# Kernel optimization log

Measured on AMD Instinct MI355X. Metric: run time of the kernel, lower is better.

Reference implementation:

```python
import jax, jax.numpy as jnp
import numpy as np

B, S, D, H = 2, 2048, 1024, 16
DH = D // H  # per-head dim (64)


def setup_inputs() -> dict:
    key = jax.random.key(0)
    ks = jax.random.split(key, 12)
    scale = 1.0 / np.sqrt(D)
    return {
        "q": jax.random.normal(ks[0], (B, S, D), jnp.float32),
        "k": jax.random.normal(ks[1], (B, S, D), jnp.float32),
        "v": jax.random.normal(ks[2], (B, S, D), jnp.float32),
        # per-head projection weights, stacked: head i's nn.Linear(d_model, d)
        "Wq": jax.random.normal(ks[3], (H, D, DH), jnp.float32) * scale,
        "Wk": jax.random.normal(ks[4], (H, D, DH), jnp.float32) * scale,
        "Wv": jax.random.normal(ks[5], (H, D, DH), jnp.float32) * scale,
        "bq": jax.random.normal(ks[6], (H, DH), jnp.float32) * scale,
        "bk": jax.random.normal(ks[7], (H, DH), jnp.float32) * scale,
        "bv": jax.random.normal(ks[8], (H, DH), jnp.float32) * scale,
        # output projection nn.Linear(d_model, d_model)
        "Wo": jax.random.normal(ks[9], (D, D), jnp.float32) * scale,
        "bo": jax.random.normal(ks[10], (D,), jnp.float32) * scale,
    }


def reference(q, k, v, Wq, Wk, Wv, bq, bk, bv, Wo, bo):
    # Per-head projections (batched over heads): [B, S, H, DH]
    Q = jnp.einsum("bsd,hdk->bshk", q, Wq) + bq
    K = jnp.einsum("bsd,hdk->bshk", k, Wk) + bk
    V = jnp.einsum("bsd,hdk->bshk", v, Wv) + bv
    # Scaled dot-product attention per head: scores [B, H, S, S]
    scores = jnp.einsum("bqhk,bvhk->bhqv", Q, K) / jnp.sqrt(jnp.float32(DH))
    aw = jax.nn.softmax(scores, axis=-1)  # attention weights
    # Weighted values, concat heads along last dim (head i -> slice i*DH:(i+1)*DH)
    ctx = jnp.einsum("bhqv,bvhk->bqhk", aw, V).reshape(B, S, D)
    out = ctx @ Wo + bo  # dropout is identity in eval
    # aws stacked over heads first, matching torch.stack: [H, B, S, S]
    aws = jnp.transpose(aw, (1, 0, 2, 3))
    return out, aws
```

## Files before the change

kernel.cpp:

```cpp
#include <hip/hip_runtime.h>
#include <hip/hip_bf16.h>
#include <cstdint>
#include <cstddef>

#define B_  2
#define S_  2048
#define D_  1024
#define H_  16
#define DH_ 64
#define OUT_ELEMS ((size_t)B_ * S_ * D_)

typedef unsigned short u16;
typedef __attribute__((ext_vector_type(8))) short short8;
typedef __attribute__((ext_vector_type(4))) float f32x4;

__device__ __forceinline__ float bf2f(u16 u) {
    union { unsigned int i; float f; } x;
    x.i = ((unsigned int)u) << 16;
    return x.f;
}
__device__ __forceinline__ u16 f2bf(float f) {
    union { float f; unsigned int i; } x; x.f = f;
    unsigned int r = x.i + 0x7fffu + ((x.i >> 16) & 1u);
    return (u16)(r >> 16);
}

#define LDSTR 72

__global__ __launch_bounds__(64) void detect_kernel(const void* q, unsigned int* flag)
{
    const int lane = threadIdx.x;
    const u16 e = ((const u16*)q)[lane * 2];
    const float v = bf2f(e);
    const float a = fabsf(v);
    const bool wild = !(a <= 100.f) || (a != 0.f && a < 1e-6f);
    unsigned long long m = __ballot(wild);
    if (lane == 0) *flag = (__popcll(m) >= 16) ? 1u : 0u;
}

__global__ __launch_bounds__(256) void convert_bias_kernel(
    const void* bq, const void* bk, const void* bv, const void* bo,
    u16* __restrict__ dst, const unsigned int* __restrict__ flag)
{
    const bool ext32 = flag[0] != 0;
    const int which = blockIdx.y;
    const void* src = which == 0 ? bq : which == 1 ? bk : which == 2 ? bv : bo;
    u16* d = dst + which * 1024;
    const int tid = threadIdx.x;
    #pragma unroll
    for (int i = 0; i < 4; ++i) {
        const int idx = i * 256 + tid;
        d[idx] = ext32 ? f2bf(((const float*)src)[idx]) : ((const u16*)src)[idx];
    }
}

__global__ __launch_bounds__(256) void transpose_weights_kernel(
    const void* Wq, const void* Wk, const void* Wv, const void* Wo,
    u16* __restrict__ WqT, u16* __restrict__ WkT,
    u16* __restrict__ WvT, u16* __restrict__ WoT,
    const unsigned int* __restrict__ flag)
{
    __shared__ u16 t[64][65];
    const bool ext32 = flag[0] != 0;
    const int which = blockIdx.y;
    const void* src = which == 0 ? Wq : which == 1 ? Wk : which == 2 ? Wv : Wo;
    u16* dst = which == 0 ? WqT : which == 1 ? WkT : which == 2 ? WvT : WoT;
    const int tile = blockIdx.x;
    const int tid = threadIdx.x;
    const int rr = tid >> 6;
    const int cc = tid & 63;

    if (which < 3) {
        const int h = tile >> 4, d0 = (tile & 15) * 64;
        #pragma unroll
        for (int i = 0; i < 16; ++i) {
            int r = rr + i * 4;
            size_t idx = ((size_t)(h * 1024 + d0 + r)) * 64 + cc;
            t[r][cc] = ext32 ? f2bf(((const float*)src)[idx]) : ((const u16*)src)[idx];
        }
        __syncthreads();
        #pragma unroll
        for (int i = 0; i < 16; ++i) {
            int c = rr + i * 4;
            dst[((size_t)(h * 64 + c)) * 1024 + d0 + cc] = t[cc][c];
        }
    } else {
        const int d0 = (tile >> 4) * 64, n0 = (tile & 15) * 64;
        #pragma unroll
        for (int i = 0; i < 16; ++i) {
            int r = rr + i * 4;
            size_t idx = (size_t)(d0 + r) * 1024 + n0 + cc;
            t[r][cc] = ext32 ? f2bf(((const float*)src)[idx]) : ((const u16*)src)[idx];
        }
        __syncthreads();
        #pragma unroll
        for (int i = 0; i < 16; ++i) {
            int c = rr + i * 4;
            dst[(size_t)(n0 + c) * 1024 + d0 + cc] = t[cc][c];
        }
    }
}

__global__ __launch_bounds__(256) void gemm_bias_kernel(
    const void* __restrict__ A, const u16* __restrict__ BT,
    const u16* __restrict__ bias, void* __restrict__ out,
    int M, int K, int mode, int a_ext, const unsigned int* __restrict__ flag)
{
    __shared__ u16 lA[128 * LDSTR];
    __shared__ u16 lB[128 * LDSTR];
    const bool ext32 = flag[0] != 0;
    const int tid = threadIdx.x;
    const int wave = tid >> 6, lane = tid & 63;
    const int m0 = blockIdx.x * 128, n0 = blockIdx.y * 128;
    const int wm = (wave >> 1) * 64, wn = (wave & 1) * 64;

    f32x4 acc[4][4];
    #pragma unroll
    for (int i = 0; i < 4; ++i)
        #pragma unroll
        for (int j = 0; j < 4; ++j)
            acc[i][j] = (f32x4){0.f, 0.f, 0.f, 0.f};

    for (int k0 = 0; k0 < K; k0 += 64) {
        if (a_ext && ext32) {
            const float* Af = (const float*)A;
            #pragma unroll
            for (int it = 0; it < 4; ++it) {
                int e = (it * 256 + tid) * 8;
                int r = e >> 6, c = e & 63;
                const float4 f0 = *(const float4*)&Af[(size_t)(m0 + r) * K + k0 + c];
                const float4 f1 = *(const float4*)&Af[(size_t)(m0 + r) * K + k0 + c + 4];
                short8 o;
                o[0] = (short)f2bf(f0.x); o[1] = (short)f2bf(f0.y);
                o[2] = (short)f2bf(f0.z); o[3] = (short)f2bf(f0.w);
                o[4] = (short)f2bf(f1.x); o[5] = (short)f2bf(f1.y);
                o[6] = (short)f2bf(f1.z); o[7] = (short)f2bf(f1.w);
                *(short8*)&lA[r * LDSTR + c] = o;
                *(short8*)&lB[r * LDSTR + c] = *(const short8*)&BT[(size_t)(n0 + r) * K + k0 + c];
            }
        } else {
            const u16* Ab = (const u16*)A;
            #pragma unroll
            for (int it = 0; it < 4; ++it) {
                int e = (it * 256 + tid) * 8;
                int r = e >> 6, c = e & 63;
                *(short8*)&lA[r * LDSTR + c] = *(const short8*)&Ab[(size_t)(m0 + r) * K + k0 + c];
                *(short8*)&lB[r * LDSTR + c] = *(const short8*)&BT[(size_t)(n0 + r) * K + k0 + c];
            }
        }
        __syncthreads();
        #pragma unroll
        for (int ks = 0; ks < 2; ++ks) {
            const int fk = ((lane >> 4) << 3) + ks * 32;
            const int fr = lane & 15;
            short8 af[4], bf[4];
            #pragma unroll
            for (int i = 0; i < 4; ++i) af[i] = *(short8*)&lA[(wm + i * 16 + fr) * LDSTR + fk];
            #pragma unroll
            for (int j = 0; j < 4; ++j) bf[j] = *(short8*)&lB[(wn + j * 16 + fr) * LDSTR + fk];
            #pragma unroll
            for (int i = 0; i < 4; ++i)
                #pragma unroll
                for (int j = 0; j < 4; ++j)
                    acc[i][j] = __builtin_amdgcn_mfma_f32_16x16x32_bf16(af[i], bf[j], acc[i][j], 0, 0, 0);
        }
        __syncthreads();
    }

    const int cf = lane & 15;
    const int rb = (lane >> 4) * 4;
    #pragma unroll
    for (int j = 0; j < 4; ++j) {
        const int n = n0 + wn + j * 16 + cf;
        const float bval = bf2f(bias[n]);
        const int h = n >> 6, dh = n & 63;
        #pragma unroll
        for (int i = 0; i < 4; ++i) {
            #pragma unroll
            for (int reg = 0; reg < 4; ++reg) {
                const int m = m0 + wm + i * 16 + rb + reg;
                const float v = acc[i][j][reg] + bval;
                if (mode == 0) {
                    int b = m >> 11, s = m & (S_ - 1);
                    ((u16*)out)[((size_t)(b * H_ + h) * S_ + s) * DH_ + dh] = f2bf(v);
                } else if (mode == 1) {
                    int b = m >> 11, s = m & (S_ - 1);
                    ((u16*)out)[((size_t)(b * H_ + h) * DH_ + dh) * S_ + s] = f2bf(v);
                } else {
                    size_t off = (size_t)m * D_ + n;
                    if (ext32) ((float*)out)[off] = v;
                    else       ((u16*)out)[off] = f2bf(v);
                }
            }
        }
    }
}

template<int WITH_PV>
__global__ __launch_bounds__(256, 3) void fused_attn_kernel(
    const u16* __restrict__ Qp, const u16* __restrict__ Kp,
    const u16* __restrict__ Vt, void* __restrict__ dout,
    u16* __restrict__ ctx, const unsigned int* __restrict__ flag)
{
    __shared__ u16 lQ[64 * LDSTR];
    __shared__ u16 lK[64 * LDSTR];
    __shared__ u16 lV[WITH_PV ? 64 * LDSTR : 8];
    __shared__ u16 lP[WITH_PV ? 4 * 16 * LDSTR : 8];

    const bool ext32 = flag[0] != 0;
    const int tid = threadIdx.x;
    const int wave = tid >> 6, lane = tid & 63;
    const int lin = blockIdx.x;
    const int g = lin & 7, ii = lin >> 3;
    const int bh = g * 4 + (ii & 3);
    const int mblk = ii >> 2;
    const int b = bh >> 4, h = bh & 15;
    const int m0 = mblk * 64;
    const int wm = wave * 16;
    const int fr = lane & 15;
    const int quad = lane >> 4;
    const int fk = quad * 8;

    const u16* Qb = Qp + (size_t)bh * S_ * DH_;
    const u16* Kb = Kp + (size_t)bh * S_ * DH_;
    const u16* Vb = Vt + (size_t)bh * DH_ * S_;

    #pragma unroll
    for (int it = 0; it < 2; ++it) {
        int e = (it * 256 + tid) * 8;
        int r = e >> 6, c = e & 63;
        *(short8*)&lQ[r * LDSTR + c] = *(const short8*)&Qb[(size_t)(m0 + r) * DH_ + c];
    }
    __syncthreads();
    short8 aq[2];
    aq[0] = *(short8*)&lQ[(wm + fr) * LDSTR + fk];
    aq[1] = *(short8*)&lQ[(wm + fr) * LDSTR + fk + 32];

    float mrun[4], lrun[4];
    #pragma unroll
    for (int r = 0; r < 4; ++r) { mrun[r] = -1e30f; lrun[r] = 0.f; }

    for (int kt = 0; kt < S_ / 64; ++kt) {
        #pragma unroll
        for (int it = 0; it < 2; ++it) {
            int e = (it * 256 + tid) * 8;
            int r = e >> 6, c = e & 63;
            *(short8*)&lK[r * LDSTR + c] = *(const short8*)&Kb[(size_t)(kt * 64 + r) * DH_ + c];
        }
        __syncthreads();
        f32x4 sacc[4];
        #pragma unroll
        for (int j = 0; j < 4; ++j) sacc[j] = (f32x4){0.f, 0.f, 0.f, 0.f};
        #pragma unroll
        for (int ks = 0; ks < 2; ++ks)
            #pragma unroll
            for (int j = 0; j < 4; ++j) {
                short8 bk = *(short8*)&lK[(j * 16 + fr) * LDSTR + fk + ks * 32];
                sacc[j] = __builtin_amdgcn_mfma_f32_16x16x32_bf16(aq[ks], bk, sacc[j], 0, 0, 0);
            }
        __syncthreads();

        #pragma unroll
        for (int r = 0; r < 4; ++r) {
            float pm = fmaxf(fmaxf(sacc[0][r], sacc[1][r]), fmaxf(sacc[2][r], sacc[3][r]));
            #pragma unroll
            for (int off = 1; off < 16; off <<= 1) pm = fmaxf(pm, __shfl_xor(pm, off, 64));
            const float mnew = fmaxf(mrun[r], pm * 0.125f);
            float t = 0.f;
            #pragma unroll
            for (int j = 0; j < 4; ++j)
                t += __expf(fmaf(sacc[j][r], 0.125f, -mnew));
            #pragma unroll
            for (int off = 1; off < 16; off <<= 1) t += __shfl_xor(t, off, 64);
            lrun[r] = lrun[r] * __expf(mrun[r] - mnew) + t;
            mrun[r] = mnew;
        }
    }

    float inv[4];
    #pragma unroll
    for (int r = 0; r < 4; ++r) inv[r] = 1.f / lrun[r];

    f32x4 pv[4];
    if (WITH_PV) {
        #pragma unroll
        for (int j = 0; j < 4; ++j) pv[j] = (f32x4){0.f, 0.f, 0.f, 0.f};
    }

    float* awF = (float*)dout + OUT_ELEMS + (size_t)(h * B_ + b) * S_ * S_;
    u16*  awH = (u16*)dout + OUT_ELEMS + (size_t)(h * B_ + b) * S_ * S_;

    for (int kt = 0; kt < S_ / 64; ++kt) {
        #pragma unroll
        for (int it = 0; it < 2; ++it) {
            int e = (it * 256 + tid) * 8;
            int r = e >> 6, c = e & 63;
            *(short8*)&lK[r * LDSTR + c] = *(const short8*)&Kb[(size_t)(kt * 64 + r) * DH_ + c];
            if (WITH_PV)
                *(short8*)&lV[r * LDSTR + c] = *(const short8*)&Vb[(size_t)r * S_ + kt * 64 + c];
        }
        __syncthreads();
        f32x4 sacc[4];
        #pragma unroll
        for (int j = 0; j < 4; ++j) sacc[j] = (f32x4){0.f, 0.f, 0.f, 0.f};
        #pragma unroll
        for (int ks = 0; ks < 2; ++ks)
            #pragma unroll
            for (int j = 0; j < 4; ++j) {
                short8 bk = *(short8*)&lK[(j * 16 + fr) * LDSTR + fk + ks * 32];
                sacc[j] = __builtin_amdgcn_mfma_f32_16x16x32_bf16(aq[ks], bk, sacc[j], 0, 0, 0);
            }

        #pragma unroll
        for (int j = 0; j < 4; ++j) {
            const int col = kt * 64 + j * 16 + fr;
            #pragma unroll
            for (int r = 0; r < 4; ++r) {
                const float p = __expf(fmaf(sacc[j][r], 0.125f, -mrun[r])) * inv[r];
                const int row = m0 + wm + quad * 4 + r;
                if (ext32) awF[(size_t)row * S_ + col] = p;
                else       awH[(size_t)row * S_ + col] = f2bf(p);
                if (WITH_PV) lP[(wm + quad * 4 + r) * LDSTR + j * 16 + fr] = f2bf(p);
            }
        }
        if (WITH_PV) {
            asm volatile("s_waitcnt lgkmcnt(0)" ::: "memory");
            __builtin_amdgcn_sched_barrier(0);
            #pragma unroll
            for (int ks = 0; ks < 2; ++ks) {
                short8 ap = *(short8*)&lP[(wm + fr) * LDSTR + fk + ks * 32];
                #pragma unroll
                for (int j = 0; j < 4; ++j) {
                    short8 bv = *(short8*)&lV[(j * 16 + fr) * LDSTR + fk + ks * 32];
                    pv[j] = __builtin_amdgcn_mfma_f32_16x16x32_bf16(ap, bv, pv[j], 0, 0, 0);
                }
            }
        }
        __syncthreads();
    }

    if (WITH_PV) {
        #pragma unroll
        for (int j = 0; j < 4; ++j) {
            const int dh = j * 16 + fr;
            #pragma unroll
            for (int r = 0; r < 4; ++r) {
                const int mrow = m0 + wm + quad * 4 + r;
                ctx[((size_t)(b * S_ + mrow)) * D_ + h * DH_ + dh] = f2bf(pv[j][r]);
            }
        }
    }
}

__global__ __launch_bounds__(128) void ctx_kernel(
    const void* __restrict__ dout, const u16* __restrict__ Vt, u16* __restrict__ ctx,
    const unsigned int* __restrict__ flag)
{
    __shared__ u16 lA[128 * LDSTR];
    __shared__ u16 lB[64 * LDSTR];
    const bool ext32 = flag[0] != 0;
    const int tid = threadIdx.x;
    const int wave = tid >> 6, lane = tid & 63;
    const int bh = blockIdx.z, b = bh >> 4, h = bh & 15;
    const int m0 = blockIdx.x * 128;
    const int wm = wave * 64;
    const size_t abase = (size_t)(h * B_ + b) * S_ * S_;
    const u16* Bv = Vt + (size_t)bh * DH_ * S_;

    f32x4 acc[4][4];
    #pragma unroll
    for (int i = 0; i < 4; ++i)
        #pragma unroll
        for (int j = 0; j < 4; ++j)
            acc[i][j] = (f32x4){0.f, 0.f, 0.f, 0.f};

    for (int k0 = 0; k0 < S_; k0 += 64) {
        if (ext32) {
            const float* Awf = (const float*)dout + OUT_ELEMS + abase;
            #pragma unroll
            for (int it = 0; it < 8; ++it) {
                int e = (it * 128 + tid) * 8;
                int r = e >> 6, c = e & 63;
                const float4 f0 = *(const float4*)&Awf[(size_t)(m0 + r) * S_ + k0 + c];
                const float4 f1 = *(const float4*)&Awf[(size_t)(m0 + r) * S_ + k0 + c + 4];
                short8 o;
                o[0] = (short)f2bf(f0.x); o[1] = (short)f2bf(f0.y);
                o[2] = (short)f2bf(f0.z); o[3] = (short)f2bf(f0.w);
                o[4] = (short)f2bf(f1.x); o[5] = (short)f2bf(f1.y);
                o[6] = (short)f2bf(f1.z); o[7] = (short)f2bf(f1.w);
                *(short8*)&lA[r * LDSTR + c] = o;
            }
        } else {
            const u16* Awb = (const u16*)dout + OUT_ELEMS + abase;
            #pragma unroll
            for (int it = 0; it < 8; ++it) {
                int e = (it * 128 + tid) * 8;
                int r = e >> 6, c = e & 63;
                *(short8*)&lA[r * LDSTR + c] = *(const short8*)&Awb[(size_t)(m0 + r) * S_ + k0 + c];
            }
        }
        #pragma unroll
        for (int it = 0; it < 4; ++it) {
            int e = (it * 128 + tid) * 8;
            int r = e >> 6, c = e & 63;
            *(short8*)&lB[r * LDSTR + c] = *(const short8*)&Bv[(size_t)r * S_ + k0 + c];
        }
        __syncthreads();
        #pragma unroll
        for (int ks = 0; ks < 2; ++ks) {
            const int fk = ((lane >> 4) << 3) + ks * 32;
            const int fr = lane & 15;
            short8 af[4], bf[4];
            #pragma unroll
            for (int i = 0; i < 4; ++i) af[i] = *(short8*)&lA[(wm + i * 16 + fr) * LDSTR + fk];
            #pragma unroll
            for (int j = 0; j < 4; ++j) bf[j] = *(short8*)&lB[(j * 16 + fr) * LDSTR + fk];
            #pragma unroll
            for (int i = 0; i < 4; ++i)
                #pragma unroll
                for (int j = 0; j < 4; ++j)
                    acc[i][j] = __builtin_amdgcn_mfma_f32_16x16x32_bf16(af[i], bf[j], acc[i][j], 0, 0, 0);
        }
        __syncthreads();
    }

    const int cf = lane & 15;
    const int rb = (lane >> 4) * 4;
    #pragma unroll
    for (int j = 0; j < 4; ++j) {
        const int n = j * 16 + cf;
        #pragma unroll
        for (int i = 0; i < 4; ++i) {
            #pragma unroll
            for (int reg = 0; reg < 4; ++reg) {
                const int m = m0 + wm + i * 16 + rb + reg;
                ctx[((size_t)(b * S_ + m)) * D_ + h * DH_ + n] = f2bf(acc[i][j][reg]);
            }
        }
    }
}

extern "C" void kernel_launch(void* const* d_in, const int* in_sizes, int n_in,
                              void* d_out, int out_size, void* d_ws, size_t ws_size,
                              hipStream_t stream)
{
    const void* q  = d_in[0];
    const void* k  = d_in[1];
    const void* v  = d_in[2];
    const void* Wq = d_in[3];
    const void* Wk = d_in[4];
    const void* Wv = d_in[5];
    const void* bq = d_in[6];
    const void* bk = d_in[7];
    const void* bv = d_in[8];
    const void* Wo = d_in[9];
    const void* bo = d_in[10];

    u16* ws   = (u16*)d_ws;
    u16* WqT  = ws;
    u16* WkT  = ws + 1048576;
    u16* WvT  = ws + 2097152;
    u16* WoT  = ws + 3145728;
    u16* Qp   = ws + 4194304;
    u16* Kp   = ws + 8388608;
    u16* Vt   = ws + 12582912;
    u16* biasB = ws + 16777216;
    unsigned int* flag = (unsigned int*)(ws + 16781312);
    u16* ctxws = ws + 16781376;

    const bool big_ws = ws_size >= (size_t)(16781376 + 4194304) * sizeof(u16);
    u16* ctxbuf = big_ws ? ctxws : Qp;

    detect_kernel<<<1, 64, 0, stream>>>(q, flag);
    convert_bias_kernel<<<dim3(1, 4), 256, 0, stream>>>(bq, bk, bv, bo, biasB, flag);
    transpose_weights_kernel<<<dim3(256, 4), 256, 0, stream>>>(
        Wq, Wk, Wv, Wo, WqT, WkT, WvT, WoT, flag);
    gemm_bias_kernel<<<dim3(32, 8), 256, 0, stream>>>(q, WqT, biasB,        Qp, 4096, 1024, 0, 1, flag);
    gemm_bias_kernel<<<dim3(32, 8), 256, 0, stream>>>(k, WkT, biasB + 1024, Kp, 4096, 1024, 0, 1, flag);
    gemm_bias_kernel<<<dim3(32, 8), 256, 0, stream>>>(v, WvT, biasB + 2048, Vt, 4096, 1024, 1, 1, flag);

    if (big_ws) {
        fused_attn_kernel<1><<<dim3(1024), 256, 0, stream>>>(Qp, Kp, Vt, d_out, ctxws, flag);
    } else {
        fused_attn_kernel<0><<<dim3(1024), 256, 0, stream>>>(Qp, Kp, Vt, d_out, nullptr, flag);
        ctx_kernel<<<dim3(16, 1, 32), 128, 0, stream>>>(d_out, Vt, Qp, flag);
    }
    gemm_bias_kernel<<<dim3(32, 8), 256, 0, stream>>>(ctxbuf, WoT, biasB + 3072, d_out, 4096, 1024, 2, 0, flag);
}
```

Before: 859.5 us.

## Merge QKV projections into one launch, stage epilogue through LDS, defer softmax reductions

Replaces the three separate Q/K/V projection GEMM launches with one 3D-grid kernel. Its epilogue now goes through LDS, so global writes are coalesced 16-byte stores, including the transposed V layout that used to be written as strided 2-byte scalar stores. The first softmax pass keeps per-lane running max and sum, and combines them across lanes with shuffles only once after the loop, removing the per-tile shuffle reductions. The attention kernel also reuses the Q LDS buffer for P to shrink shared memory, which may raise occupancy. The cost is extra LDS traffic and a barrier in the GEMM epilogue, plus a slightly more complex merge of lane statistics.

```diff
diff --git a/kernel.cpp b/kernel.cpp
--- a/kernel.cpp
+++ b/kernel.cpp
@@ -26,6 +26,7 @@
 }
 
 #define LDSTR 72
+#define LDTR  136
 
 __global__ __launch_bounds__(64) void detect_kernel(const void* q, unsigned int* flag)
 {
@@ -101,18 +102,26 @@
     }
 }
 
-__global__ __launch_bounds__(256) void gemm_bias_kernel(
-    const void* __restrict__ A, const u16* __restrict__ BT,
-    const u16* __restrict__ bias, void* __restrict__ out,
-    int M, int K, int mode, int a_ext, const unsigned int* __restrict__ flag)
-{
-    __shared__ u16 lA[128 * LDSTR];
-    __shared__ u16 lB[128 * LDSTR];
+__global__ __launch_bounds__(256) void qkv_gemm_kernel(
+    const void* __restrict__ qin, const void* __restrict__ kin, const void* __restrict__ vin,
+    const u16* __restrict__ WqT, const u16* __restrict__ WkT, const u16* __restrict__ WvT,
+    const u16* __restrict__ biasB,
+    u16* __restrict__ Qp, u16* __restrict__ Kp, u16* __restrict__ Vt,
+    const unsigned int* __restrict__ flag)
+{
+    __shared__ u16 lds[2 * 128 * LDSTR];
+    u16* lA = lds;
+    u16* lB = lds + 128 * LDSTR;
     const bool ext32 = flag[0] != 0;
+    const int z = blockIdx.z;
+    const void* A = z == 0 ? qin : z == 1 ? kin : vin;
+    const u16* BT = z == 0 ? WqT : z == 1 ? WkT : WvT;
+    const u16* bias = biasB + z * 1024;
     const int tid = threadIdx.x;
     const int wave = tid >> 6, lane = tid & 63;
     const int m0 = blockIdx.x * 128, n0 = blockIdx.y * 128;
     const int wm = (wave >> 1) * 64, wn = (wave & 1) * 64;
+    const int K = 1024;
 
     f32x4 acc[4][4];
     #pragma unroll
@@ -122,7 +131,7 @@
             acc[i][j] = (f32x4){0.f, 0.f, 0.f, 0.f};
 
     for (int k0 = 0; k0 < K; k0 += 64) {
-        if (a_ext && ext32) {
+        if (ext32) {
             const float* Af = (const float*)A;
             #pragma unroll
             for (int it = 0; it < 4; ++it) {
@@ -167,30 +176,122 @@
         __syncthreads();
     }
 
+    u16* lT = lds;
+    const int cf = lane & 15;
+    const int rb = (lane >> 4) * 4;
+    if (z < 2) {
+        #pragma unroll
+        for (int j = 0; j < 4; ++j) {
+            const int nl = wn + j * 16 + cf;
+            const float bval = bf2f(bias[n0 + nl]);
+            #pragma unroll
+            for (int i = 0; i < 4; ++i)
+                #pragma unroll
+                for (int reg = 0; reg < 4; ++reg) {
+                    const int ml = wm + i * 16 + rb + reg;
+                    lT[ml * LDTR + nl] = f2bf(acc[i][j][reg] + bval);
+                }
+        }
+        __syncthreads();
+        u16* out = z == 0 ? Qp : Kp;
+        #pragma unroll
+        for (int it = 0; it < 8; ++it) {
+            const int idx = (it * 256 + tid) * 8;
+            const int row = idx >> 7, col = idx & 127;
+            const int m = m0 + row, n = n0 + col;
+            const int b = m >> 11, s = m & (S_ - 1), h = n >> 6, dh = n & 63;
+            *(short8*)&out[((size_t)(b * H_ + h) * S_ + s) * DH_ + dh] =
+                *(const short8*)&lT[row * LDTR + col];
+        }
+    } else {
+        #pragma unroll
+        for (int j = 0; j < 4; ++j) {
+            const int nl = wn + j * 16 + cf;
+            const float bval = bf2f(bias[n0 + nl]);
+            #pragma unroll
+            for (int i = 0; i < 4; ++i)
+                #pragma unroll
+                for (int reg = 0; reg < 4; ++reg) {
+                    const int ml = wm + i * 16 + rb + reg;
+                    lT[nl * LDTR + ml] = f2bf(acc[i][j][reg] + bval);
+                }
+        }
+        __syncthreads();
+        #pragma unroll
+        for (int it = 0; it < 8; ++it) {
+            const int idx = (it * 256 + tid) * 8;
+            const int row = idx >> 7, col = idx & 127;
+            const int n = n0 + row, m = m0 + col;
+            const int b = m >> 11, s = m & (S_ - 1), h = n >> 6, dh = n & 63;
+            *(short8*)&Vt[((size_t)(b * H_ + h) * DH_ + dh) * S_ + s] =
+                *(const short8*)&lT[row * LDTR + col];
+        }
+    }
+}
+
+__global__ __launch_bounds__(256) void gemm_bias_kernel(
+    const void* __restrict__ A, const u16* __restrict__ BT,
+    const u16* __restrict__ bias, void* __restrict__ out,
+    int M, int K, const unsigned int* __restrict__ flag)
+{
+    __shared__ u16 lA[128 * LDSTR];
+    __shared__ u16 lB[128 * LDSTR];
+    const bool ext32 = flag[0] != 0;
+    const int tid = threadIdx.x;
+    const int wave = tid >> 6, lane = tid & 63;
+    const int m0 = blockIdx.x * 128, n0 = blockIdx.y * 128;
+    const int wm = (wave >> 1) * 64, wn = (wave & 1) * 64;
+
+    f32x4 acc[4][4];
+    #pragma unroll
+    for (int i = 0; i < 4; ++i)
+        #pragma unroll
+        for (int j = 0; j < 4; ++j)
+            acc[i][j] = (f32x4){0.f, 0.f, 0.f, 0.f};
+
+    for (int k0 = 0; k0 < K; k0 += 64) {
+        const u16* Ab = (const u16*)A;
+        #pragma unroll
+        for (int it = 0; it < 4; ++it) {
+            int e = (it * 256 + tid) * 8;
+            int r = e >> 6, c = e & 63;
+            *(short8*)&lA[r * LDSTR + c] = *(const short8*)&Ab[(size_t)(m0 + r) * K + k0 + c];
+            *(short8*)&lB[r * LDSTR + c] = *(const short8*)&BT[(size_t)(n0 + r) * K + k0 + c];
+        }
+        __syncthreads();
+        #pragma unroll
+        for (int ks = 0; ks < 2; ++ks) {
+            const int fk = ((lane >> 4) << 3) + ks * 32;
+            const int fr = lane & 15;
+            short8 af[4], bf[4];
+            #pragma unroll
+            for (int i = 0; i < 4; ++i) af[i] = *(short8*)&lA[(wm + i * 16 + fr) * LDSTR + fk];
+            #pragma unroll
+            for (int j = 0; j < 4; ++j) bf[j] = *(short8*)&lB[(wn + j * 16 + fr) * LDSTR + fk];
+            #pragma unroll
+            for (int i = 0; i < 4; ++i)
+                #pragma unroll
+                for (int j = 0; j < 4; ++j)
+                    acc[i][j] = __builtin_amdgcn_mfma_f32_16x16x32_bf16(af[i], bf[j], acc[i][j], 0, 0, 0);
+        }
+        __syncthreads();
+    }
+
     const int cf = lane & 15;
     const int rb = (lane >> 4) * 4;
     #pragma unroll
     for (int j = 0; j < 4; ++j) {
         const int n = n0 + wn + j * 16 + cf;
         const float bval = bf2f(bias[n]);
-        const int h = n >> 6, dh = n & 63;
         #pragma unroll
         for (int i = 0; i < 4; ++i) {
             #pragma unroll
             for (int reg = 0; reg < 4; ++reg) {
                 const int m = m0 + wm + i * 16 + rb + reg;
                 const float v = acc[i][j][reg] + bval;
-                if (mode == 0) {
-                    int b = m >> 11, s = m & (S_ - 1);
-                    ((u16*)out)[((size_t)(b * H_ + h) * S_ + s) * DH_ + dh] = f2bf(v);
-                } else if (mode == 1) {
-                    int b = m >> 11, s = m & (S_ - 1);
-                    ((u16*)out)[((size_t)(b * H_ + h) * DH_ + dh) * S_ + s] = f2bf(v);
-                } else {
-                    size_t off = (size_t)m * D_ + n;
-                    if (ext32) ((float*)out)[off] = v;
-                    else       ((u16*)out)[off] = f2bf(v);
-                }
+                size_t off = (size_t)m * D_ + n;
+                if (ext32) ((float*)out)[off] = v;
+                else       ((u16*)out)[off] = f2bf(v);
             }
         }
     }
@@ -202,10 +303,10 @@
     const u16* __restrict__ Vt, void* __restrict__ dout,
     u16* __restrict__ ctx, const unsigned int* __restrict__ flag)
 {
-    __shared__ u16 lQ[64 * LDSTR];
-    __shared__ u16 lK[64 * LDSTR];
-    __shared__ u16 lV[WITH_PV ? 64 * LDSTR : 8];
-    __shared__ u16 lP[WITH_PV ? 4 * 16 * LDSTR : 8];
+    __shared__ u16 sh[(WITH_PV ? 3 : 2) * 64 * LDSTR];
+    u16* lK  = sh;
+    u16* lQP = sh + 64 * LDSTR;
+    u16* lV  = WITH_PV ? sh + 2 * 64 * LDSTR : sh;
 
     const bool ext32 = flag[0] != 0;
     const int tid = threadIdx.x;
@@ -229,12 +330,12 @@
     for (int it = 0; it < 2; ++it) {
         int e = (it * 256 + tid) * 8;
         int r = e >> 6, c = e & 63;
-        *(short8*)&lQ[r * LDSTR + c] = *(const short8*)&Qb[(size_t)(m0 + r) * DH_ + c];
+        *(short8*)&lQP[r * LDSTR + c] = *(const short8*)&Qb[(size_t)(m0 + r) * DH_ + c];
     }
     __syncthreads();
     short8 aq[2];
-    aq[0] = *(short8*)&lQ[(wm + fr) * LDSTR + fk];
-    aq[1] = *(short8*)&lQ[(wm + fr) * LDSTR + fk + 32];
+    aq[0] = *(short8*)&lQP[(wm + fr) * LDSTR + fk];
+    aq[1] = *(short8*)&lQP[(wm + fr) * LDSTR + fk + 32];
 
     float mrun[4], lrun[4];
     #pragma unroll
@@ -262,16 +363,13 @@
 
         #pragma unroll
         for (int r = 0; r < 4; ++r) {
-            float pm = fmaxf(fmaxf(sacc[0][r], sacc[1][r]), fmaxf(sacc[2][r], sacc[3][r]));
-            #pragma unroll
-            for (int off = 1; off < 16; off <<= 1) pm = fmaxf(pm, __shfl_xor(pm, off, 64));
-            const float mnew = fmaxf(mrun[r], pm * 0.125f);
-            float t = 0.f;
-            #pragma unroll
-            for (int j = 0; j < 4; ++j)
-                t += __expf(fmaf(sacc[j][r], 0.125f, -mnew));
-            #pragma unroll
-            for (int off = 1; off < 16; off <<= 1) t += __shfl_xor(t, off, 64);
+            const float pm = fmaxf(fmaxf(sacc[0][r], sacc[1][r]),
+                                   fmaxf(sacc[2][r], sacc[3][r])) * 0.125f;
+            const float mnew = fmaxf(mrun[r], pm);
+            float t = __expf(fmaf(sacc[0][r], 0.125f, -mnew))
+                    + __expf(fmaf(sacc[1][r], 0.125f, -mnew))
+                    + __expf(fmaf(sacc[2][r], 0.125f, -mnew))
+                    + __expf(fmaf(sacc[3][r], 0.125f, -mnew));
             lrun[r] = lrun[r] * __expf(mrun[r] - mnew) + t;
             mrun[r] = mnew;
         }
@@ -279,7 +377,17 @@
 
     float inv[4];
     #pragma unroll
-    for (int r = 0; r < 4; ++r) inv[r] = 1.f / lrun[r];
+    for (int r = 0; r < 4; ++r) {
+        #pragma unroll
+        for (int off = 1; off < 16; off <<= 1) {
+            const float mo = __shfl_xor(mrun[r], off, 64);
+            const float lo = __shfl_xor(lrun[r], off, 64);
+            const float mn = fmaxf(mrun[r], mo);
+            lrun[r] = lrun[r] * __expf(mrun[r] - mn) + lo * __expf(mo - mn);
+            mrun[r] = mn;
+        }
+        inv[r] = 1.f / lrun[r];
+    }
 
     f32x4 pv[4];
     if (WITH_PV) {
@@ -320,7 +428,7 @@
                 const int row = m0 + wm + quad * 4 + r;
                 if (ext32) awF[(size_t)row * S_ + col] = p;
                 else       awH[(size_t)row * S_ + col] = f2bf(p);
-                if (WITH_PV) lP[(wm + quad * 4 + r) * LDSTR + j * 16 + fr] = f2bf(p);
+                if (WITH_PV) lQP[(wm + quad * 4 + r) * LDSTR + j * 16 + fr] = f2bf(p);
             }
         }
         if (WITH_PV) {
@@ -328,7 +436,7 @@
             __builtin_amdgcn_sched_barrier(0);
             #pragma unroll
             for (int ks = 0; ks < 2; ++ks) {
-                short8 ap = *(short8*)&lP[(wm + fr) * LDSTR + fk + ks * 32];
+                short8 ap = *(short8*)&lQP[(wm + fr) * LDSTR + fk + ks * 32];
                 #pragma unroll
                 for (int j = 0; j < 4; ++j) {
                     short8 bv = *(short8*)&lV[(j * 16 + fr) * LDSTR + fk + ks * 32];
@@ -475,9 +583,8 @@
     convert_bias_kernel<<<dim3(1, 4), 256, 0, stream>>>(bq, bk, bv, bo, biasB, flag);
     transpose_weights_kernel<<<dim3(256, 4), 256, 0, stream>>>(
         Wq, Wk, Wv, Wo, WqT, WkT, WvT, WoT, flag);
-    gemm_bias_kernel<<<dim3(32, 8), 256, 0, stream>>>(q, WqT, biasB,        Qp, 4096, 1024, 0, 1, flag);
-    gemm_bias_kernel<<<dim3(32, 8), 256, 0, stream>>>(k, WkT, biasB + 1024, Kp, 4096, 1024, 0, 1, flag);
-    gemm_bias_kernel<<<dim3(32, 8), 256, 0, stream>>>(v, WvT, biasB + 2048, Vt, 4096, 1024, 1, 1, flag);
+    qkv_gemm_kernel<<<dim3(32, 8, 3), 256, 0, stream>>>(
+        q, k, v, WqT, WkT, WvT, biasB, Qp, Kp, Vt, flag);
 
     if (big_ws) {
         fused_attn_kernel<1><<<dim3(1024), 256, 0, stream>>>(Qp, Kp, Vt, d_out, ctxws, flag);
@@ -485,5 +592,5 @@
         fused_attn_kernel<0><<<dim3(1024), 256, 0, stream>>>(Qp, Kp, Vt, d_out, nullptr, flag);
         ctx_kernel<<<dim3(16, 1, 32), 128, 0, stream>>>(d_out, Vt, Qp, flag);
     }
-    gemm_bias_kernel<<<dim3(32, 8), 256, 0, stream>>>(ctxbuf, WoT, biasB + 3072, d_out, 4096, 1024, 2, 0, flag);
-}
+    gemm_bias_kernel<<<dim3(32, 8), 256, 0, stream>>>(ctxbuf, WoT, biasB + 3072, d_out, 4096, 1024, flag);
+}
```

New measurement: 799.2 us. -7.0%, faster.
